# Kernel tuning notes

Hardware: AMD Instinct MI355X
Metric: run time of the kernel (lower is better)

The kernel has to match this reference:

```python
import jax, jax.numpy as jnp
import numpy as np

NEG_SLOPE = 0.2  # PyG GATConv default negative_slope
N_NODES = 4096
N_EDGES = 32768
IN_CH = 128
HID = 512
OUT_CH = 10
HEADS = 8


def gat_conv(x, src, dst, W, a_src, a_dst, bias, num_nodes):
    """PyG-style GATConv (eval mode, self-loops already in src/dst).
    x: [N, F_in], W: [F_in, H*C], a_src/a_dst: [H, C], bias: [H*C].
    Returns concat-heads output [N, H*C]."""
    H, C = a_src.shape
    h = (x @ W).reshape(num_nodes, H, C)                      # [N,H,C]
    alpha_src = jnp.sum(h * a_src, axis=-1)                   # [N,H]
    alpha_dst = jnp.sum(h * a_dst, axis=-1)                   # [N,H]
    e = alpha_src[src] + alpha_dst[dst]                       # [E,H] per-edge logits
    e = jnp.where(e > 0, e, NEG_SLOPE * e)                    # leaky_relu
    # segment softmax over incoming edges of each dst node (self-loops => non-empty)
    m = jax.ops.segment_max(e, dst, num_segments=num_nodes)   # [N,H]
    e = jnp.exp(e - m[dst])
    denom = jax.ops.segment_sum(e, dst, num_segments=num_nodes)
    alpha = e / denom[dst]                                    # [E,H]
    msg = h[src] * alpha[:, :, None]                          # [E,H,C] gather+weight
    out = jax.ops.segment_sum(msg, dst, num_segments=num_nodes)  # scatter-add
    return out.reshape(num_nodes, H * C) + bias


def setup_inputs() -> dict:
    key = jax.random.key(0)
    ks = jax.random.split(key, 16)
    s = 0.05
    inp = {
        "x": jax.random.normal(ks[0], (N_NODES, IN_CH), jnp.float32),
        "edge_index": jax.random.randint(ks[1], (2, N_EDGES), 0, N_NODES, jnp.int64),
        "edge_attr": jax.random.normal(ks[2], (N_EDGES, 16), jnp.float32),
        "W1": jax.random.normal(ks[3], (IN_CH, HEADS * HID), jnp.float32) * s,
        "a_src1": jax.random.normal(ks[4], (HEADS, HID), jnp.float32) * s,
        "a_dst1": jax.random.normal(ks[5], (HEADS, HID), jnp.float32) * s,
        "b1": jnp.zeros((HEADS * HID,), jnp.float32),
        "W2": jax.random.normal(ks[6], (HEADS * HID, HID), jnp.float32) * s,
        "a_src2": jax.random.normal(ks[7], (1, HID), jnp.float32) * s,
        "a_dst2": jax.random.normal(ks[8], (1, HID), jnp.float32) * s,
        "b2": jnp.zeros((HID,), jnp.float32),
        # MLP head
        "fc1_w": jax.random.normal(ks[9], (4096, 512), jnp.float32) * s,
        "fc1_b": jnp.zeros((512,), jnp.float32),
        "fc2_w": jax.random.normal(ks[10], (512, 128), jnp.float32) * s,
        "fc2_b": jnp.zeros((128,), jnp.float32),
        "fc3_w": jax.random.normal(ks[11], (128, OUT_CH), jnp.float32) * s,
        "fc3_b": jnp.zeros((OUT_CH,), jnp.float32),
    }
    return inp


def reference(x, edge_index, edge_attr, W1, a_src1, a_dst1, b1, W2, a_src2, a_dst2, b2,
              fc1_w, fc1_b, fc2_w, fc2_b, fc3_w, fc3_b):
    # edge_attr is ignored: GATConv was built without edge_dim (lin_edge is None in PyG).
    del edge_attr
    n = x.shape[0]
    loops = jnp.arange(n, dtype=edge_index.dtype)
    src = jnp.concatenate([edge_index[0], loops])  # add_self_loops=True default
    dst = jnp.concatenate([edge_index[1], loops])
    h = jax.nn.relu(gat_conv(x, src, dst, W1, a_src1, a_dst1, b1, n))   # [N, 4096]
    h = jax.nn.relu(gat_conv(h, src, dst, W2, a_src2, a_dst2, b2, n))   # [N, 512]
    g = h.reshape(-1, 8 * h.shape[-1])                                   # [N/8, 4096]
    g = jax.nn.relu(g @ fc1_w + fc1_b)
    g = jax.nn.relu(g @ fc2_w + fc2_b)
    return g @ fc3_w + fc3_b                                             # [N/8, 10]
```

## Files before the change

kernel.cpp:

```cpp
#include <hip/hip_runtime.h>
#include <cstdint>
#include <cstddef>

#define NN    4096
#define E0C   32768
#define ETC   (E0C+NN)
#define HC1   8
#define CC    512
#define F_IN  128
#define NEG_SLOPE_F 0.2f

typedef __bf16 bf16_t;
typedef __bf16 bf16x8 __attribute__((ext_vector_type(8)));
typedef __bf16 bf16x4 __attribute__((ext_vector_type(4)));
typedef float  f32x4  __attribute__((ext_vector_type(4)));

__device__ __forceinline__ void tcast_body(const float* __restrict__ W, bf16_t* __restrict__ Wt,
                                           int K, int N, int bx, int by)
{
    __shared__ float t[32][33];
    int bn = bx * 32, bk = by * 32;
    int tx = threadIdx.x & 31, ty = threadIdx.x >> 5;
    #pragma unroll
    for (int i = 0; i < 32; i += 8)
        t[ty + i][tx] = W[(size_t)(bk + ty + i) * N + bn + tx];
    __syncthreads();
    #pragma unroll
    for (int i = 0; i < 32; i += 8)
        Wt[(size_t)(bn + ty + i) * K + bk + tx] = (bf16_t)t[tx][ty + i];
}

__global__ __launch_bounds__(256) void prep_k(const float* __restrict__ x,
    const float* __restrict__ W1, const float* __restrict__ W2,
    const float* __restrict__ fc1w, const float* __restrict__ a_src1,
    const float* __restrict__ a_dst1,
    bf16_t* __restrict__ x_bf, bf16_t* __restrict__ Wt1, bf16_t* __restrict__ Wt2,
    bf16_t* __restrict__ fc1wt, bf16_t* __restrict__ w1sT)
{
    const int b = blockIdx.x;
    if (b < 512) {
        int i = (b * 256 + threadIdx.x) * 4;
        float4 v = *(const float4*)&x[i];
        bf16x4 o;
        o[0] = (bf16_t)v.x; o[1] = (bf16_t)v.y; o[2] = (bf16_t)v.z; o[3] = (bf16_t)v.w;
        *(bf16x4*)&x_bf[i] = o;
    } else if (b < 1024) {
        int bl = b - 512;
        tcast_body(W1, Wt1, F_IN, 4096, bl % 128, bl / 128);
    } else if (b < 3072) {
        int bl = b - 1024;
        tcast_body(W2, Wt2, 4096, 512, bl % 16, bl / 16);
    } else if (b < 5120) {
        int bl = b - 3072;
        tcast_body(fc1w, fc1wt, 4096, 512, bl % 16, bl / 16);
    } else {
        int bl = b - 5120;
        int wave = threadIdx.x >> 6, lane = threadIdx.x & 63;
        int k = bl * 4 + wave;
        int hd = lane >> 3;
        int co = (lane & 7) * 64;
        const float* wrow = W1 + (size_t)k * (HC1 * CC) + hd * CC + co;
        const float* vs = a_src1 + hd * CC + co;
        const float* vd = a_dst1 + hd * CC + co;
        float s = 0.f, d = 0.f;
        #pragma unroll 4
        for (int t = 0; t < 64; ++t) {
            float w = wrow[t];
            s += w * vs[t];
            d += w * vd[t];
        }
        #pragma unroll
        for (int off = 1; off < 8; off <<= 1) {
            s += __shfl_xor(s, off);
            d += __shfl_xor(d, off);
        }
        if ((lane & 7) == 0) {
            w1sT[hd * F_IN + k]       = (bf16_t)s;
            w1sT[(hd + 8) * F_IN + k] = (bf16_t)d;
        }
    }
}

__global__ __launch_bounds__(64) void alpha1_k(const bf16_t* __restrict__ x_bf,
                                               const bf16_t* __restrict__ w1sT,
                                               float* __restrict__ as1, float* __restrict__ ad1)
{
    const int bm = blockIdx.x * 16;
    const int lane = threadIdx.x;
    const int lm = lane & 15, quad = lane >> 4;
    f32x4 acc = {};
    #pragma unroll
    for (int k0 = 0; k0 < F_IN; k0 += 32) {
        bf16x8 af = *(const bf16x8*)&x_bf[(size_t)(bm + lm) * F_IN + k0 + quad * 8];
        bf16x8 bf = *(const bf16x8*)&w1sT[lm * F_IN + k0 + quad * 8];
        acc = __builtin_amdgcn_mfma_f32_16x16x32_bf16(af, bf, acc, 0, 0, 0);
    }
    #pragma unroll
    for (int r = 0; r < 4; ++r) {
        int n = bm + quad * 4 + r;
        if (lm < 8) as1[n * HC1 + lm] = acc[r];
        else        ad1[n * HC1 + (lm - 8)] = acc[r];
    }
}

template<typename OutT, bool RELU, bool HASBIAS, bool SPLIT>
__global__ __launch_bounds__(256, 2) void gemm128_k(const bf16_t* __restrict__ A,
                                                    const bf16_t* __restrict__ Bt,
                                                    const float* __restrict__ bias,
                                                    OutT* __restrict__ Cout,
                                                    float* __restrict__ Cpart,
                                                    int M, int N, int K, int Kc)
{
    __shared__ bf16_t As[128 * 32];
    __shared__ bf16_t Bs[128 * 32];
    const int tid = threadIdx.x;
    const int bm = blockIdx.x * 128, bn = blockIdx.y * 128;
    const int kz = blockIdx.z;
    const int k_beg = kz * Kc;
    const int k_end = k_beg + Kc;

    const int wave = tid >> 6, lane = tid & 63;
    const int wm = wave >> 1, wn = wave & 1;
    const int lm = lane & 15, quad = lane >> 4;

    const int sr = tid >> 2;
    const int kg = tid & 3;
    const int swz = ((kg ^ (sr & 3)) * 8);

    const bf16_t* Aptr = A + (size_t)(bm + sr) * K + k_beg + kg * 8;
    const bf16_t* Bptr = Bt + (size_t)(bn + sr) * K + k_beg + kg * 8;
    const size_t rowskip = (size_t)64 * K;

    bf16x8 ra0 = *(const bf16x8*)(Aptr);
    bf16x8 ra1 = *(const bf16x8*)(Aptr + rowskip);
    bf16x8 rb0 = *(const bf16x8*)(Bptr);
    bf16x8 rb1 = *(const bf16x8*)(Bptr + rowskip);

    f32x4 acc[4][4] = {};

    for (int k0 = k_beg; k0 < k_end; k0 += 32) {
        __syncthreads();
        *(bf16x8*)&As[sr * 32 + swz]        = ra0;
        *(bf16x8*)&As[(sr + 64) * 32 + swz] = ra1;
        *(bf16x8*)&Bs[sr * 32 + swz]        = rb0;
        *(bf16x8*)&Bs[(sr + 64) * 32 + swz] = rb1;
        __syncthreads();
        if (k0 + 32 < k_end) {
            Aptr += 32; Bptr += 32;
            ra0 = *(const bf16x8*)(Aptr);
            ra1 = *(const bf16x8*)(Aptr + rowskip);
            rb0 = *(const bf16x8*)(Bptr);
            rb1 = *(const bf16x8*)(Bptr + rowskip);
        }
        const int fswz = ((quad ^ (lm & 3)) * 8);
        bf16x8 af[4], bfr[4];
        #pragma unroll
        for (int i = 0; i < 4; ++i) {
            af[i]  = *(const bf16x8*)&As[(wm * 64 + i * 16 + lm) * 32 + fswz];
            bfr[i] = *(const bf16x8*)&Bs[(wn * 64 + i * 16 + lm) * 32 + fswz];
        }
        #pragma unroll
        for (int mt = 0; mt < 4; ++mt)
            #pragma unroll
            for (int nt = 0; nt < 4; ++nt)
                acc[mt][nt] = __builtin_amdgcn_mfma_f32_16x16x32_bf16(af[mt], bfr[nt], acc[mt][nt], 0, 0, 0);
    }

    if (SPLIT) {
        float* P = Cpart + (size_t)kz * M * N;
        #pragma unroll
        for (int nt = 0; nt < 4; ++nt) {
            int gc = bn + wn * 64 + nt * 16 + lm;
            #pragma unroll
            for (int mt = 0; mt < 4; ++mt)
                #pragma unroll
                for (int r = 0; r < 4; ++r) {
                    int gr = bm + wm * 64 + mt * 16 + quad * 4 + r;
                    P[(size_t)gr * N + gc] = acc[mt][nt][r];
                }
        }
    } else {
        #pragma unroll
        for (int nt = 0; nt < 4; ++nt) {
            int gc = bn + wn * 64 + nt * 16 + lm;
            float bv = HASBIAS ? bias[gc] : 0.f;
            #pragma unroll
            for (int mt = 0; mt < 4; ++mt)
                #pragma unroll
                for (int r = 0; r < 4; ++r) {
                    int gr = bm + wm * 64 + mt * 16 + quad * 4 + r;
                    float v = acc[mt][nt][r] + bv;
                    if (RELU) v = fmaxf(v, 0.f);
                    Cout[(size_t)gr * N + gc] = (OutT)v;
                }
        }
    }
}

template<typename OutT, bool RELU, bool HASBIAS>
__global__ void reduce_split_k(const float* __restrict__ P, const float* __restrict__ bias,
                               OutT* __restrict__ Cout, int MN, int N, int S)
{
    int i = (blockIdx.x * 256 + threadIdx.x) * 4;
    if (i >= MN) return;
    f32x4 s = *(const f32x4*)&P[i];
    for (int z = 1; z < S; ++z)
        s += *(const f32x4*)&P[(size_t)z * MN + i];
    int col = i % N;
    #pragma unroll
    for (int j = 0; j < 4; ++j) {
        float v = s[j];
        if (HASBIAS) v += bias[col + j];
        if (RELU) v = fmaxf(v, 0.f);
        Cout[i + j] = (OutT)v;
    }
}

__global__ __launch_bounds__(256) void reduce_h2_k(const float* __restrict__ P,
    const float* __restrict__ a_s, const float* __restrict__ a_d,
    bf16_t* __restrict__ h2bf, float* __restrict__ as2, float* __restrict__ ad2)
{
    const int t = threadIdx.x;
    const int i = (blockIdx.x * 256 + t) * 4;
    f32x4 s = *(const f32x4*)&P[i];
    #pragma unroll
    for (int z = 1; z < 4; ++z)
        s += *(const f32x4*)&P[(size_t)z * NN * CC + i];
    bf16x4 o;
    #pragma unroll
    for (int j = 0; j < 4; ++j) o[j] = (bf16_t)s[j];
    *(bf16x4*)&h2bf[i] = o;
    const int c = i & (CC - 1);
    const int row = i >> 9;
    f32x4 va = *(const f32x4*)&a_s[c];
    f32x4 vd = *(const f32x4*)&a_d[c];
    float ls = s[0]*va[0] + s[1]*va[1] + s[2]*va[2] + s[3]*va[3];
    float ld = s[0]*vd[0] + s[1]*vd[1] + s[2]*vd[2] + s[3]*vd[3];
    #pragma unroll
    for (int off = 32; off > 0; off >>= 1) {
        ls += __shfl_down(ls, off);
        ld += __shfl_down(ld, off);
    }
    if ((t & 63) == 0) {
        atomicAdd(&as2[row], ls);
        atomicAdd(&ad2[row], ld);
    }
}

__global__ __launch_bounds__(128) void mlp_tail_k(const float* __restrict__ f1,
                                                  const float* __restrict__ fc2w,
                                                  const float* __restrict__ fc2b,
                                                  const float* __restrict__ fc3w,
                                                  const float* __restrict__ fc3b,
                                                  float* __restrict__ out)
{
    __shared__ float sA[512];
    __shared__ float sF2[128];
    const int m = blockIdx.x, t = threadIdx.x;
    #pragma unroll
    for (int i = 0; i < 4; ++i) sA[t + i * 128] = f1[(size_t)m * 512 + t + i * 128];
    __syncthreads();
    float a0 = 0.f, a1 = 0.f, a2 = 0.f, a3 = 0.f;
    #pragma unroll 4
    for (int k = 0; k < 512; k += 4) {
        a0 += sA[k + 0] * fc2w[(k + 0) * 128 + t];
        a1 += sA[k + 1] * fc2w[(k + 1) * 128 + t];
        a2 += sA[k + 2] * fc2w[(k + 2) * 128 + t];
        a3 += sA[k + 3] * fc2w[(k + 3) * 128 + t];
    }
    sF2[t] = fmaxf((a0 + a1) + (a2 + a3) + fc2b[t], 0.f);
    __syncthreads();
    if (t < 10) {
        float o = fc3b[t];
        #pragma unroll 4
        for (int k = 0; k < 128; ++k)
            o += sF2[k] * fc3w[k * 10 + t];
        out[(size_t)m * 10 + t] = o;
    }
}

__global__ void build_edges_k(const int* __restrict__ ei, int* __restrict__ srcA,
                              int* __restrict__ dstA, int* __restrict__ indeg)
{
    int e = blockIdx.x * 256 + threadIdx.x;
    if (e >= ETC) return;
    int s, d;
    if (e < E0C) { s = ei[e]; d = ei[E0C + e]; }
    else         { s = e - E0C; d = s; }
    srcA[e] = s; dstA[e] = d;
    atomicAdd(&indeg[d], 1);
}

__global__ void scan_k(const int* __restrict__ indeg, int* __restrict__ offs)
{
    __shared__ int part[1024];
    int t = threadIdx.x;
    int v0 = indeg[t*4+0], v1 = indeg[t*4+1], v2 = indeg[t*4+2], v3 = indeg[t*4+3];
    int sum = v0 + v1 + v2 + v3;
    part[t] = sum;
    __syncthreads();
    for (int off = 1; off < 1024; off <<= 1) {
        int x = (t >= off) ? part[t - off] : 0;
        __syncthreads();
        part[t] += x;
        __syncthreads();
    }
    int excl = part[t] - sum;
    offs[t*4+0] = excl;
    offs[t*4+1] = excl + v0;
    offs[t*4+2] = excl + v0 + v1;
    offs[t*4+3] = excl + v0 + v1 + v2;
    if (t == 1023) offs[4096] = excl + sum;
}

__global__ void fill_csr_k(const int* __restrict__ srcA, const int* __restrict__ dstA,
                           const int* __restrict__ offs, int* __restrict__ cursor,
                           int* __restrict__ epos, int* __restrict__ srcCSR)
{
    int e = blockIdx.x * 256 + threadIdx.x;
    if (e >= ETC) return;
    int d = dstA[e];
    int pos = atomicAdd(&cursor[d], 1);
    int slot = offs[d] + pos;
    epos[e] = slot;
    srcCSR[slot] = srcA[e];
}

template<int H>
__global__ void edge_fused_k(const int* __restrict__ srcA, const int* __restrict__ dstA,
                             const int* __restrict__ epos,
                             const float* __restrict__ as, const float* __restrict__ ad,
                             float* __restrict__ pCSR, float* __restrict__ denom)
{
    int idx = blockIdx.x * 256 + threadIdx.x;
    if (idx >= ETC * H) return;
    int e = idx / H, hd = idx - e * H;
    int s = srcA[e], d = dstA[e];
    float v = as[s*H + hd] + ad[d*H + hd];
    v = (v > 0.f) ? v : NEG_SLOPE_F * v;
    float p = __expf(v);
    pCSR[(size_t)hd * ETC + epos[e]] = p;
    atomicAdd(&denom[d*H + hd], p);
}

template<int H>
__global__ __launch_bounds__(256) void aggregate_k(const bf16_t* __restrict__ hbuf,
    const float* __restrict__ pCSR, const float* __restrict__ denom,
    const int* __restrict__ offs, const int* __restrict__ srcCSR,
    const float* __restrict__ bias, bf16_t* __restrict__ outb)
{
    const int b = blockIdx.x;
    const int hd = b % H;
    const int g  = b / H;
    const int wave = threadIdx.x >> 6, lane = threadIdx.x & 63;
    const int n = g * 4 + wave;
    const int c = lane * 8;

    const int beg = offs[n], end = offs[n + 1];
    const int deg = end - beg;
    const float inv = 1.f / denom[n * H + hd];

    float acc[8] = {};
    for (int base = 0; base < deg; base += 64) {
        int idx = base + lane;
        int vsrc = 0; float vp = 0.f;
        if (idx < deg) {
            vsrc = srcCSR[beg + idx];
            vp   = pCSR[(size_t)hd * ETC + beg + idx] * inv;
        }
        int cnt = min(deg - base, 64);
        int ii = 0;
        for (; ii + 4 <= cnt; ii += 4) {
            int s0 = __shfl(vsrc, ii),     s1 = __shfl(vsrc, ii + 1);
            int s2 = __shfl(vsrc, ii + 2), s3 = __shfl(vsrc, ii + 3);
            float a0 = __shfl(vp, ii),     a1 = __shfl(vp, ii + 1);
            float a2 = __shfl(vp, ii + 2), a3 = __shfl(vp, ii + 3);
            bf16x8 r0 = *(const bf16x8*)&hbuf[((size_t)s0 * H + hd) * CC + c];
            bf16x8 r1 = *(const bf16x8*)&hbuf[((size_t)s1 * H + hd) * CC + c];
            bf16x8 r2 = *(const bf16x8*)&hbuf[((size_t)s2 * H + hd) * CC + c];
            bf16x8 r3 = *(const bf16x8*)&hbuf[((size_t)s3 * H + hd) * CC + c];
            #pragma unroll
            for (int j = 0; j < 8; ++j) {
                acc[j] += a0 * (float)r0[j];
                acc[j] += a1 * (float)r1[j];
                acc[j] += a2 * (float)r2[j];
                acc[j] += a3 * (float)r3[j];
            }
        }
        for (; ii < cnt; ++ii) {
            int s = __shfl(vsrc, ii);
            float al = __shfl(vp, ii);
            bf16x8 rv = *(const bf16x8*)&hbuf[((size_t)s * H + hd) * CC + c];
            #pragma unroll
            for (int j = 0; j < 8; ++j)
                acc[j] += al * (float)rv[j];
        }
    }
    size_t ob = ((size_t)n * H + hd) * CC;
    bf16x8 o;
    #pragma unroll
    for (int j = 0; j < 8; ++j)
        o[j] = (bf16_t)fmaxf(acc[j] + bias[hd * CC + c + j], 0.f);
    *(bf16x8*)&outb[ob + c] = o;
}

extern "C" void kernel_launch(void* const* d_in, const int* in_sizes, int n_in,
                              void* d_out, int out_size, void* d_ws, size_t ws_size,
                              hipStream_t stream) {
    const float* x      = (const float*)d_in[0];
    const int*   ei     = (const int*)d_in[1];
    const float* W1     = (const float*)d_in[3];
    const float* a_src1 = (const float*)d_in[4];
    const float* a_dst1 = (const float*)d_in[5];
    const float* b1     = (const float*)d_in[6];
    const float* W2     = (const float*)d_in[7];
    const float* a_src2 = (const float*)d_in[8];
    const float* a_dst2 = (const float*)d_in[9];
    const float* b2     = (const float*)d_in[10];
    const float* fc1w   = (const float*)d_in[11];
    const float* fc1b   = (const float*)d_in[12];
    const float* fc2w   = (const float*)d_in[13];
    const float* fc2b   = (const float*)d_in[14];
    const float* fc3w   = (const float*)d_in[15];
    const float* fc3b   = (const float*)d_in[16];
    float* out = (float*)d_out;

    char* ws = (char*)d_ws;
    size_t o = 0;
    auto take = [&](size_t bytes) -> char* {
        char* p = ws + o;
        o = (o + bytes + 255) & ~(size_t)255;
        return p;
    };
    int*    indeg  = (int*)take(NN * 4);
    int*    cursor = (int*)take(NN * 4);
    float*  dn1    = (float*)take((size_t)NN * HC1 * 4);
    float*  dn2    = (float*)take(NN * 4);
    float*  as2    = (float*)take(NN * 4);
    float*  ad2    = (float*)take(NN * 4);
    size_t zero_bytes = o;
    int*    offs   = (int*)take((NN + 1) * 4);
    int*    srcA   = (int*)take(ETC * 4);
    int*    dstA   = (int*)take(ETC * 4);
    int*    epos   = (int*)take(ETC * 4);
    int*    srcCSR = (int*)take(ETC * 4);
    float*  p1     = (float*)take((size_t)ETC * HC1 * 4);
    float*  p2     = (float*)take(ETC * 4);
    float*  as1    = (float*)take((size_t)NN * HC1 * 4);
    float*  ad1    = (float*)take((size_t)NN * HC1 * 4);
    bf16_t* w1sT   = (bf16_t*)take((size_t)16 * F_IN * 2);
    bf16_t* x_bf   = (bf16_t*)take((size_t)NN * F_IN * 2);
    bf16_t* Wt1    = (bf16_t*)take((size_t)F_IN * 4096 * 2);
    bf16_t* Wt2    = (bf16_t*)take((size_t)4096 * 512 * 2);
    bf16_t* fc1wt  = (bf16_t*)take((size_t)4096 * 512 * 2);
    bf16_t* h1bf   = (bf16_t*)take((size_t)NN * 4096 * 2);
    bf16_t* out1bf = (bf16_t*)take((size_t)NN * 4096 * 2);
    bf16_t* h2bf   = (bf16_t*)take((size_t)NN * 512 * 2);
    bf16_t* out2bf = (bf16_t*)take((size_t)NN * 512 * 2);
    float*  f1     = (float*)take((size_t)512 * 512 * 4);
    float*  part   = (float*)take((size_t)4 * NN * 512 * 4);

    hipMemsetAsync(d_ws, 0, zero_bytes, stream);

    build_edges_k<<<dim3((ETC + 255) / 256), dim3(256), 0, stream>>>(ei, srcA, dstA, indeg);
    scan_k<<<dim3(1), dim3(1024), 0, stream>>>(indeg, offs);
    fill_csr_k<<<dim3((ETC + 255) / 256), dim3(256), 0, stream>>>(srcA, dstA, offs, cursor, epos, srcCSR);

    prep_k<<<dim3(5152), dim3(256), 0, stream>>>(x, W1, W2, fc1w, a_src1, a_dst1,
                                                 x_bf, Wt1, Wt2, fc1wt, w1sT);

    gemm128_k<bf16_t, false, false, false><<<dim3(32, 32, 1), dim3(256), 0, stream>>>(
        x_bf, Wt1, nullptr, h1bf, nullptr, 4096, 4096, F_IN, F_IN);
    alpha1_k<<<dim3(NN / 16), dim3(64), 0, stream>>>(x_bf, w1sT, as1, ad1);
    edge_fused_k<HC1><<<dim3((ETC * HC1 + 255) / 256), dim3(256), 0, stream>>>(
        srcA, dstA, epos, as1, ad1, p1, dn1);
    aggregate_k<HC1><<<dim3(NN / 4 * HC1), dim3(256), 0, stream>>>(
        h1bf, p1, dn1, offs, srcCSR, b1, out1bf);

    gemm128_k<float, false, false, true><<<dim3(32, 4, 4), dim3(256), 0, stream>>>(
        out1bf, Wt2, nullptr, nullptr, part, 4096, 512, 4096, 1024);
    reduce_h2_k<<<dim3(NN * 512 / 1024), dim3(256), 0, stream>>>(
        part, a_src2, a_dst2, h2bf, as2, ad2);
    edge_fused_k<1><<<dim3((ETC + 255) / 256), dim3(256), 0, stream>>>(
        srcA, dstA, epos, as2, ad2, p2, dn2);
    aggregate_k<1><<<dim3(NN / 4), dim3(256), 0, stream>>>(
        h2bf, p2, dn2, offs, srcCSR, b2, out2bf);

    gemm128_k<float, false, false, true><<<dim3(4, 4, 16), dim3(256), 0, stream>>>(
        out2bf, fc1wt, nullptr, nullptr, part, 512, 512, 4096, 256);
    reduce_split_k<float, true, true><<<dim3(512 * 512 / 4 / 256), dim3(256), 0, stream>>>(
        part, fc1b, f1, 512 * 512, 512, 16);
    mlp_tail_k<<<dim3(512), dim3(128), 0, stream>>>(f1, fc2w, fc2b, fc3w, fc3b, out);
}
```

Baseline: 252.6 us.

## Fuse edge softmax into aggregation and fold edge build into prep kernel

```diff
diff --git a/kernel.cpp b/kernel.cpp
--- a/kernel.cpp
+++ b/kernel.cpp
@@ -33,9 +33,10 @@
 __global__ __launch_bounds__(256) void prep_k(const float* __restrict__ x,
     const float* __restrict__ W1, const float* __restrict__ W2,
     const float* __restrict__ fc1w, const float* __restrict__ a_src1,
-    const float* __restrict__ a_dst1,
+    const float* __restrict__ a_dst1, const int* __restrict__ ei,
     bf16_t* __restrict__ x_bf, bf16_t* __restrict__ Wt1, bf16_t* __restrict__ Wt2,
-    bf16_t* __restrict__ fc1wt, bf16_t* __restrict__ w1sT)
+    bf16_t* __restrict__ fc1wt, bf16_t* __restrict__ w1sT,
+    int* __restrict__ srcA, int* __restrict__ dstA, int* __restrict__ indeg)
 {
     const int b = blockIdx.x;
     if (b < 512) {
@@ -53,7 +54,7 @@
     } else if (b < 5120) {
         int bl = b - 3072;
         tcast_body(fc1w, fc1wt, 4096, 512, bl % 16, bl / 16);
-    } else {
+    } else if (b < 5152) {
         int bl = b - 5120;
         int wave = threadIdx.x >> 6, lane = threadIdx.x & 63;
         int k = bl * 4 + wave;
@@ -78,6 +79,15 @@
             w1sT[hd * F_IN + k]       = (bf16_t)s;
             w1sT[(hd + 8) * F_IN + k] = (bf16_t)d;
         }
+    } else {
+        int e = (b - 5152) * 256 + threadIdx.x;
+        if (e < ETC) {
+            int s, d;
+            if (e < E0C) { s = ei[e]; d = ei[E0C + e]; }
+            else         { s = e - E0C; d = s; }
+            srcA[e] = s; dstA[e] = d;
+            atomicAdd(&indeg[d], 1);
+        }
     }
 }
 
@@ -279,18 +289,6 @@
     }
 }
 
-__global__ void build_edges_k(const int* __restrict__ ei, int* __restrict__ srcA,
-                              int* __restrict__ dstA, int* __restrict__ indeg)
-{
-    int e = blockIdx.x * 256 + threadIdx.x;
-    if (e >= ETC) return;
-    int s, d;
-    if (e < E0C) { s = ei[e]; d = ei[E0C + e]; }
-    else         { s = e - E0C; d = s; }
-    srcA[e] = s; dstA[e] = d;
-    atomicAdd(&indeg[d], 1);
-}
-
 __global__ void scan_k(const int* __restrict__ indeg, int* __restrict__ offs)
 {
     __shared__ int part[1024];
@@ -315,37 +313,18 @@
 
 __global__ void fill_csr_k(const int* __restrict__ srcA, const int* __restrict__ dstA,
                            const int* __restrict__ offs, int* __restrict__ cursor,
-                           int* __restrict__ epos, int* __restrict__ srcCSR)
+                           int* __restrict__ srcCSR)
 {
     int e = blockIdx.x * 256 + threadIdx.x;
     if (e >= ETC) return;
     int d = dstA[e];
     int pos = atomicAdd(&cursor[d], 1);
-    int slot = offs[d] + pos;
-    epos[e] = slot;
-    srcCSR[slot] = srcA[e];
-}
-
-template<int H>
-__global__ void edge_fused_k(const int* __restrict__ srcA, const int* __restrict__ dstA,
-                             const int* __restrict__ epos,
-                             const float* __restrict__ as, const float* __restrict__ ad,
-                             float* __restrict__ pCSR, float* __restrict__ denom)
-{
-    int idx = blockIdx.x * 256 + threadIdx.x;
-    if (idx >= ETC * H) return;
-    int e = idx / H, hd = idx - e * H;
-    int s = srcA[e], d = dstA[e];
-    float v = as[s*H + hd] + ad[d*H + hd];
-    v = (v > 0.f) ? v : NEG_SLOPE_F * v;
-    float p = __expf(v);
-    pCSR[(size_t)hd * ETC + epos[e]] = p;
-    atomicAdd(&denom[d*H + hd], p);
+    srcCSR[offs[d] + pos] = srcA[e];
 }
 
 template<int H>
 __global__ __launch_bounds__(256) void aggregate_k(const bf16_t* __restrict__ hbuf,
-    const float* __restrict__ pCSR, const float* __restrict__ denom,
+    const float* __restrict__ as, const float* __restrict__ ad,
     const int* __restrict__ offs, const int* __restrict__ srcCSR,
     const float* __restrict__ bias, bf16_t* __restrict__ outb)
 {
@@ -358,17 +337,38 @@
 
     const int beg = offs[n], end = offs[n + 1];
     const int deg = end - beg;
-    const float inv = 1.f / denom[n * H + hd];
+    const float adn = ad[n * H + hd];
+
+    int vsrc = 0; float vp = 0.f;
+    if (lane < deg) {
+        vsrc = srcCSR[beg + lane];
+        float v = as[vsrc * H + hd] + adn;
+        v = (v > 0.f) ? v : NEG_SLOPE_F * v;
+        vp = __expf(v);
+    }
+    float denom = vp;
+    #pragma unroll
+    for (int off = 1; off < 64; off <<= 1)
+        denom += __shfl_xor(denom, off);
+    for (int base = 64; base < deg; base += 64) {
+        float tp = 0.f;
+        if (base + lane < deg) {
+            int s2 = srcCSR[beg + base + lane];
+            float v = as[s2 * H + hd] + adn;
+            v = (v > 0.f) ? v : NEG_SLOPE_F * v;
+            tp = __expf(v);
+        }
+        #pragma unroll
+        for (int off = 1; off < 64; off <<= 1)
+            tp += __shfl_xor(tp, off);
+        denom += tp;
+    }
+    const float inv = 1.f / denom;
+    vp *= inv;
 
     float acc[8] = {};
-    for (int base = 0; base < deg; base += 64) {
-        int idx = base + lane;
-        int vsrc = 0; float vp = 0.f;
-        if (idx < deg) {
-            vsrc = srcCSR[beg + idx];
-            vp   = pCSR[(size_t)hd * ETC + beg + idx] * inv;
-        }
-        int cnt = min(deg - base, 64);
+    {
+        int cnt = min(deg, 64);
         int ii = 0;
         for (; ii + 4 <= cnt; ii += 4) {
             int s0 = __shfl(vsrc, ii),     s1 = __shfl(vsrc, ii + 1);
@@ -390,6 +390,25 @@
         for (; ii < cnt; ++ii) {
             int s = __shfl(vsrc, ii);
             float al = __shfl(vp, ii);
+            bf16x8 rv = *(const bf16x8*)&hbuf[((size_t)s * H + hd) * CC + c];
+            #pragma unroll
+            for (int j = 0; j < 8; ++j)
+                acc[j] += al * (float)rv[j];
+        }
+    }
+    for (int base = 64; base < deg; base += 64) {
+        int idx = base + lane;
+        int s2i = 0; float p2 = 0.f;
+        if (idx < deg) {
+            s2i = srcCSR[beg + idx];
+            float v = as[s2i * H + hd] + adn;
+            v = (v > 0.f) ? v : NEG_SLOPE_F * v;
+            p2 = __expf(v) * inv;
+        }
+        int cnt = min(deg - base, 64);
+        for (int ii = 0; ii < cnt; ++ii) {
+            int s = __shfl(s2i, ii);
+            float al = __shfl(p2, ii);
             bf16x8 rv = *(const bf16x8*)&hbuf[((size_t)s * H + hd) * CC + c];
             #pragma unroll
             for (int j = 0; j < 8; ++j)
@@ -434,18 +453,13 @@
     };
     int*    indeg  = (int*)take(NN * 4);
     int*    cursor = (int*)take(NN * 4);
-    float*  dn1    = (float*)take((size_t)NN * HC1 * 4);
-    float*  dn2    = (float*)take(NN * 4);
     float*  as2    = (float*)take(NN * 4);
     float*  ad2    = (float*)take(NN * 4);
     size_t zero_bytes = o;
     int*    offs   = (int*)take((NN + 1) * 4);
     int*    srcA   = (int*)take(ETC * 4);
     int*    dstA   = (int*)take(ETC * 4);
-    int*    epos   = (int*)take(ETC * 4);
     int*    srcCSR = (int*)take(ETC * 4);
-    float*  p1     = (float*)take((size_t)ETC * HC1 * 4);
-    float*  p2     = (float*)take(ETC * 4);
     float*  as1    = (float*)take((size_t)NN * HC1 * 4);
     float*  ad1    = (float*)take((size_t)NN * HC1 * 4);
     bf16_t* w1sT   = (bf16_t*)take((size_t)16 * F_IN * 2);
@@ -462,29 +476,24 @@
 
     hipMemsetAsync(d_ws, 0, zero_bytes, stream);
 
-    build_edges_k<<<dim3((ETC + 255) / 256), dim3(256), 0, stream>>>(ei, srcA, dstA, indeg);
+    prep_k<<<dim3(5296), dim3(256), 0, stream>>>(x, W1, W2, fc1w, a_src1, a_dst1, ei,
+                                                 x_bf, Wt1, Wt2, fc1wt, w1sT,
+                                                 srcA, dstA, indeg);
     scan_k<<<dim3(1), dim3(1024), 0, stream>>>(indeg, offs);
-    fill_csr_k<<<dim3((ETC + 255) / 256), dim3(256), 0, stream>>>(srcA, dstA, offs, cursor, epos, srcCSR);
-
-    prep_k<<<dim3(5152), dim3(256), 0, stream>>>(x, W1, W2, fc1w, a_src1, a_dst1,
-                                                 x_bf, Wt1, Wt2, fc1wt, w1sT);
+    fill_csr_k<<<dim3((ETC + 255) / 256), dim3(256), 0, stream>>>(srcA, dstA, offs, cursor, srcCSR);
 
     gemm128_k<bf16_t, false, false, false><<<dim3(32, 32, 1), dim3(256), 0, stream>>>(
         x_bf, Wt1, nullptr, h1bf, nullptr, 4096, 4096, F_IN, F_IN);
     alpha1_k<<<dim3(NN / 16), dim3(64), 0, stream>>>(x_bf, w1sT, as1, ad1);
-    edge_fused_k<HC1><<<dim3((ETC * HC1 + 255) / 256), dim3(256), 0, stream>>>(
-        srcA, dstA, epos, as1, ad1, p1, dn1);
     aggregate_k<HC1><<<dim3(NN / 4 * HC1), dim3(256), 0, stream>>>(
-        h1bf, p1, dn1, offs, srcCSR, b1, out1bf);
+        h1bf, as1, ad1, offs, srcCSR, b1, out1bf);
 
     gemm128_k<float, false, false, true><<<dim3(32, 4, 4), dim3(256), 0, stream>>>(
         out1bf, Wt2, nullptr, nullptr, part, 4096, 512, 4096, 1024);
     reduce_h2_k<<<dim3(NN * 512 / 1024), dim3(256), 0, stream>>>(
         part, a_src2, a_dst2, h2bf, as2, ad2);
-    edge_fused_k<1><<<dim3((ETC + 255) / 256), dim3(256), 0, stream>>>(
-        srcA, dstA, epos, as2, ad2, p2, dn2);
     aggregate_k<1><<<dim3(NN / 4), dim3(256), 0, stream>>>(
-        h2bf, p2, dn2, offs, srcCSR, b2, out2bf);
+        h2bf, as2, ad2, offs, srcCSR, b2, out2bf);
 
     gemm128_k<float, false, false, true><<<dim3(4, 4, 16), dim3(256), 0, stream>>>(
         out2bf, fc1wt, nullptr, nullptr, part, 512, 512, 4096, 256);
```

After: 237.2 us. 1.06x faster.
